# Optimization experiments

Measured on AMD Instinct MI355X. Metric: run time of the kernel, lower is better.

Reference implementation:

```python
import jax, jax.numpy as jnp
import numpy as np

B, N_DET, N_T, NY, NX = 4, 128, 2048, 256, 256


def setup_inputs() -> dict:
    key = jax.random.key(0)
    k1, k2, k3 = jax.random.split(key, 3)
    sino = jax.random.normal(k1, (B, 1, N_DET, N_T), dtype=jnp.float32)
    # LUT channel 0: floor temporal index (stored as float, cast to int in forward)
    k_floor = jax.random.randint(k2, (NY, NX, N_DET), 0, N_T).astype(jnp.float32)
    # LUT channel 1: linear interpolation weight alpha in [0,1)
    alpha = jax.random.uniform(k3, (NY, NX, N_DET), dtype=jnp.float32)
    lut = jnp.stack([k_floor, alpha], axis=-1)  # [NY, NX, N_DET, 2]
    return {"sino": sino, "lut": lut}


def reference(sino, lut):
    # sino: [B, 1, n_det, n_t]; lut: [ny, nx, n_det, 2]
    b, c, n_det, n_t = sino.shape
    k_floor = lut[..., 0].astype(jnp.int32)          # [ny, nx, n_det]
    alpha = lut[..., 1]                               # [ny, nx, n_det]
    valid = (k_floor >= 0) & (k_floor < n_t - 1)
    k0 = jnp.clip(k_floor, 0, n_t - 2)
    k1 = k0 + 1
    S = sino[:, 0]                                    # [B, n_det, n_t]
    det = jnp.arange(n_det)                           # broadcasts against [ny,nx,n_det]
    s0 = S[:, det, k0]                                # [B, ny, nx, n_det]
    s1 = S[:, det, k1]                                # [B, ny, nx, n_det]
    sk = (1.0 - alpha) * s0 + alpha * s1
    sk = jnp.where(valid, sk, jnp.zeros_like(sk))
    # Hann apodization window over detectors
    apod = (0.5 - 0.5 * jnp.cos(2.0 * jnp.pi * jnp.arange(n_det, dtype=jnp.float32)
                                / max(n_det - 1, 1))).astype(sino.dtype)
    out = jnp.einsum('bijd,d->bij', sk, apod)
    norm = jnp.maximum(apod.sum(), 1e-06)
    out = out / norm
    return out[:, None]                               # [B, 1, ny, nx]
```

## Files before the change

kernel.cpp:

```cpp
#include <hip/hip_runtime.h>
#include <hip/hip_fp16.h>


#define NB      4
#define NDET    128
#define NT      2048
#define NPIX    65536
#define THREADS 256

__global__ __launch_bounds__(256)
void cvt_kernel(const float* __restrict__ sino, uint2* __restrict__ ws16) {
    const int id = blockIdx.x * 256 + threadIdx.x;
    float v0 = sino[id];
    float v1 = sino[id + NDET * NT];
    float v2 = sino[id + 2 * NDET * NT];
    float v3 = sino[id + 3 * NDET * NT];
    __half2 h01 = __floats2half2_rn(v0, v1);
    __half2 h23 = __floats2half2_rn(v2, v3);
    uint2 u;
    u.x = *(const unsigned*)&h01;
    u.y = *(const unsigned*)&h23;
    ws16[id] = u;
}

__global__ __launch_bounds__(THREADS, 4)
void bp_kernel(const uint2* __restrict__ ws16,
               const float* __restrict__ lut,
               float* __restrict__ out) {
    const int tid    = threadIdx.x;
    const int lane   = tid & 63;
    const int wid    = tid >> 6;
    const int octet  = lane & 15;
    const int px_sub = lane >> 4;
    const int px     = blockIdx.x * 16 + wid * 4 + px_sub;
    const int d0     = octet * 8;

    float apod[8];
#pragma unroll
    for (int j = 0; j < 8; ++j) {
        float x = (float)(d0 + j) * (6.28318530717958647692f / 127.0f);
        apod[j] = 0.5f - 0.5f * __cosf(x);
    }

    const float4* lp = (const float4*)lut + ((size_t)px * 64 + octet * 4);
    float4 L[4];
#pragma unroll
    for (int q = 0; q < 4; ++q) L[q] = lp[q];

    float acc[NB] = {0.0f, 0.0f, 0.0f, 0.0f};
#pragma unroll
    for (int q = 0; q < 4; ++q) {
#pragma unroll
        for (int h = 0; h < 2; ++h) {
            int   j  = q * 2 + h;
            float kf = h ? L[q].z : L[q].x;
            float af = h ? L[q].w : L[q].y;
            int k = (int)kf;
            bool valid = (unsigned)k < (unsigned)(NT - 1);
            float w  = valid ? apod[j] : 0.0f;
            int  k0  = valid ? k : 0;
            const uint2* row = ws16 + (size_t)(d0 + j) * NT + k0;
            uint2 e0 = row[0];
            uint2 e1 = row[1];
            __half2 a01 = *(__half2*)&e0.x, a23 = *(__half2*)&e0.y;
            __half2 b01 = *(__half2*)&e1.x, b23 = *(__half2*)&e1.y;
            __half2 a2  = __float2half2_rn(af);
            __half2 s01 = __hfma2(a2, __hsub2(b01, a01), a01);
            __half2 s23 = __hfma2(a2, __hsub2(b23, a23), a23);
            float2 f01 = __half22float2(s01);
            float2 f23 = __half22float2(s23);
            acc[0] = fmaf(w, f01.x, acc[0]);
            acc[1] = fmaf(w, f01.y, acc[1]);
            acc[2] = fmaf(w, f23.x, acc[2]);
            acc[3] = fmaf(w, f23.y, acc[3]);
        }
    }

#pragma unroll
    for (int m = 1; m < 16; m <<= 1) {
#pragma unroll
        for (int b = 0; b < NB; ++b)
            acc[b] += __shfl_xor(acc[b], m, 64);
    }

    if (octet == 0) {
        const float inv_norm = 1.0f / 63.5f;
#pragma unroll
        for (int b = 0; b < NB; ++b)
            out[(size_t)b * NPIX + px] = acc[b] * inv_norm;
    }
}

__global__ __launch_bounds__(512, 4)
void bp_fallback(const float* __restrict__ sino,
                 const float* __restrict__ lut,
                 float* __restrict__ out) {
    __shared__ __half2 lds[4][NT];
    const int tid   = threadIdx.x;
    const int octet = blockIdx.x & 15;
    const int tile  = blockIdx.x >> 4;
    const int d0    = octet * 8;
    const int px0   = tile * 1024;
    float apod[8];
#pragma unroll
    for (int j = 0; j < 8; ++j) {
        float x = (float)(d0 + j) * (6.28318530717958647692f / 127.0f);
        apod[j] = 0.5f - 0.5f * __cosf(x);
    }
    float4 L[2][4];
#pragma unroll
    for (int i = 0; i < 2; ++i) {
        const float4* lq = (const float4*)
            (lut + ((size_t)(px0 + tid + i * 512) * NDET + d0) * 2);
#pragma unroll
        for (int q = 0; q < 4; ++q) L[i][q] = lq[q];
    }
    float acc[2][NB];
#pragma unroll
    for (int i = 0; i < 2; ++i)
#pragma unroll
        for (int b = 0; b < NB; ++b) acc[i][b] = 0.0f;
    const float4* s4 = (const float4*)sino;
    for (int ph = 0; ph < 4; ++ph) {
        const int b0  = (ph >> 1) * 2;
        const int dh  = ph & 1;
        const int dg0 = d0 + dh * 4;
        if (ph) __syncthreads();
        for (int f = tid; f < 4 * (NT / 4); f += 512) {
            int dl = f >> 9;
            int t4 = f & 511;
            size_t row = ((size_t)b0 * NDET + dg0 + dl) * (NT / 4) + t4;
            float4 ve = s4[row];
            float4 vo = s4[row + (size_t)NDET * (NT / 4)];
            __half2* dstp = &lds[dl][t4 * 4];
            dstp[0] = __floats2half2_rn(ve.x, vo.x);
            dstp[1] = __floats2half2_rn(ve.y, vo.y);
            dstp[2] = __floats2half2_rn(ve.z, vo.z);
            dstp[3] = __floats2half2_rn(ve.w, vo.w);
        }
        __syncthreads();
#pragma unroll
        for (int i = 0; i < 2; ++i) {
#pragma unroll
            for (int q2 = 0; q2 < 2; ++q2) {
                float4 Lq = L[i][dh * 2 + q2];
#pragma unroll
                for (int h = 0; h < 2; ++h) {
                    float kf = h ? Lq.z : Lq.x;
                    float af = h ? Lq.w : Lq.y;
                    int   dl = q2 * 2 + h;
                    int k = (int)kf;
                    bool valid = (unsigned)k < (unsigned)(NT - 1);
                    float w  = valid ? apod[dh * 4 + dl] : 0.0f;
                    int  k0  = valid ? k : 0;
                    __half2 s0v = lds[dl][k0];
                    __half2 s1v = lds[dl][k0 + 1];
                    __half2 a2  = __float2half2_rn(af);
                    __half2 sk  = __hfma2(a2, __hsub2(s1v, s0v), s0v);
                    float2  fv  = __half22float2(sk);
                    acc[i][b0 + 0] = fmaf(w, fv.x, acc[i][b0 + 0]);
                    acc[i][b0 + 1] = fmaf(w, fv.y, acc[i][b0 + 1]);
                }
            }
        }
    }
    const float inv_norm = 1.0f / 63.5f;
#pragma unroll
    for (int i = 0; i < 2; ++i) {
        const int px = px0 + tid + i * 512;
#pragma unroll
        for (int b = 0; b < NB; ++b)
            atomicAdd(&out[(size_t)b * NPIX + px], acc[i][b] * inv_norm);
    }
}

extern "C" void kernel_launch(void* const* d_in, const int* in_sizes, int n_in,
                              void* d_out, int out_size, void* d_ws, size_t ws_size,
                              hipStream_t stream) {
    const float* sino = (const float*)d_in[0];
    const float* lut  = (const float*)d_in[1];
    float* out = (float*)d_out;

    const size_t ws_needed = (size_t)NDET * NT * sizeof(uint2);
    if (ws_size >= ws_needed) {
        uint2* ws16 = (uint2*)d_ws;
        cvt_kernel<<<dim3(NDET * NT / 256), dim3(256), 0, stream>>>(sino, ws16);
        bp_kernel<<<dim3(NPIX / 16), dim3(THREADS), 0, stream>>>(ws16, lut, out);
    } else {
        (void)hipMemsetAsync(d_out, 0, (size_t)out_size * sizeof(float), stream);
        bp_fallback<<<dim3(1024), dim3(512), 0, stream>>>(sino, lut, out);
    }
}
```

Before: 125.9 us.

## Stage per-quad sinogram rows in LDS and accumulate detector partials atomically

The backprojection kernel is restructured so each 1024-thread block owns 4 detectors and a 4096-pixel tile. It first copies those detectors' fp16-packed sinogram rows (64KB) into shared memory, then performs the interpolation gathers from LDS instead of from global memory. Partial sums from the 32 detector groups are combined with float atomicAdd into an output that is zeroed by a memset beforehand. This replaces the warp-shuffle reduction. It aims to turn scattered L2 gathers into LDS gathers, at the cost of many atomics, a large LDS footprint that limits occupancy, and strided LUT reads.

Measured after the change: 144.3 us. +14.6%, slower.

```diff
diff --git a/kernel.cpp b/kernel.cpp
--- a/kernel.cpp
+++ b/kernel.cpp
@@ -6,7 +6,10 @@
 #define NDET    128
 #define NT      2048
 #define NPIX    65536
-#define THREADS 256
+#define QDET    4
+#define THREADS 1024
+#define PXTILE  4096
+#define ITERS   (PXTILE / THREADS)
 
 __global__ __launch_bounds__(256)
 void cvt_kernel(const float* __restrict__ sino, uint2* __restrict__ ws16) {
@@ -27,67 +30,69 @@
 void bp_kernel(const uint2* __restrict__ ws16,
                const float* __restrict__ lut,
                float* __restrict__ out) {
-    const int tid    = threadIdx.x;
-    const int lane   = tid & 63;
-    const int wid    = tid >> 6;
-    const int octet  = lane & 15;
-    const int px_sub = lane >> 4;
-    const int px     = blockIdx.x * 16 + wid * 4 + px_sub;
-    const int d0     = octet * 8;
+    __shared__ uint2 lds2[QDET * NT];
 
-    float apod[8];
+    const int tid  = threadIdx.x;
+    const int quad = blockIdx.x & 31;
+    const int tile = blockIdx.x >> 5;
+    const int d0   = quad * QDET;
+    const int px0  = tile * PXTILE;
+
+    float apod[QDET];
 #pragma unroll
-    for (int j = 0; j < 8; ++j) {
+    for (int j = 0; j < QDET; ++j) {
         float x = (float)(d0 + j) * (6.28318530717958647692f / 127.0f);
         apod[j] = 0.5f - 0.5f * __cosf(x);
     }
 
-    const float4* lp = (const float4*)lut + ((size_t)px * 64 + octet * 4);
-    float4 L[4];
+    {
+        const uint4* src = (const uint4*)(ws16 + (size_t)d0 * NT);
+        uint4* dst = (uint4*)lds2;
 #pragma unroll
-    for (int q = 0; q < 4; ++q) L[q] = lp[q];
+        for (int r = 0; r < (QDET * NT / 2) / THREADS; ++r)
+            dst[tid + r * THREADS] = src[tid + r * THREADS];
+    }
+    __syncthreads();
 
-    float acc[NB] = {0.0f, 0.0f, 0.0f, 0.0f};
+    const float inv_norm = 1.0f / 63.5f;
+
+    for (int it = 0; it < ITERS; ++it) {
+        const int px = px0 + it * THREADS + tid;
+        const float4* lp = (const float4*)(lut + ((size_t)px * NDET + d0) * 2);
+        float4 L0 = lp[0];
+        float4 L1 = lp[1];
+
+        float acc[NB] = {0.0f, 0.0f, 0.0f, 0.0f};
 #pragma unroll
-    for (int q = 0; q < 4; ++q) {
+        for (int q = 0; q < 2; ++q) {
+            float4 Lq = q ? L1 : L0;
 #pragma unroll
-        for (int h = 0; h < 2; ++h) {
-            int   j  = q * 2 + h;
-            float kf = h ? L[q].z : L[q].x;
-            float af = h ? L[q].w : L[q].y;
-            int k = (int)kf;
-            bool valid = (unsigned)k < (unsigned)(NT - 1);
-            float w  = valid ? apod[j] : 0.0f;
-            int  k0  = valid ? k : 0;
-            const uint2* row = ws16 + (size_t)(d0 + j) * NT + k0;
-            uint2 e0 = row[0];
-            uint2 e1 = row[1];
-            __half2 a01 = *(__half2*)&e0.x, a23 = *(__half2*)&e0.y;
-            __half2 b01 = *(__half2*)&e1.x, b23 = *(__half2*)&e1.y;
-            __half2 a2  = __float2half2_rn(af);
-            __half2 s01 = __hfma2(a2, __hsub2(b01, a01), a01);
-            __half2 s23 = __hfma2(a2, __hsub2(b23, a23), a23);
-            float2 f01 = __half22float2(s01);
-            float2 f23 = __half22float2(s23);
-            acc[0] = fmaf(w, f01.x, acc[0]);
-            acc[1] = fmaf(w, f01.y, acc[1]);
-            acc[2] = fmaf(w, f23.x, acc[2]);
-            acc[3] = fmaf(w, f23.y, acc[3]);
+            for (int h = 0; h < 2; ++h) {
+                int   j  = q * 2 + h;
+                float kf = h ? Lq.z : Lq.x;
+                float af = h ? Lq.w : Lq.y;
+                int k = (int)kf;
+                bool valid = (unsigned)k < (unsigned)(NT - 1);
+                float w  = valid ? apod[j] : 0.0f;
+                int  k0  = valid ? k : 0;
+                uint2 e0 = lds2[j * NT + k0];
+                uint2 e1 = lds2[j * NT + k0 + 1];
+                __half2 a01 = *(__half2*)&e0.x, a23 = *(__half2*)&e0.y;
+                __half2 b01 = *(__half2*)&e1.x, b23 = *(__half2*)&e1.y;
+                __half2 a2  = __float2half2_rn(af);
+                __half2 s01 = __hfma2(a2, __hsub2(b01, a01), a01);
+                __half2 s23 = __hfma2(a2, __hsub2(b23, a23), a23);
+                float2 f01 = __half22float2(s01);
+                float2 f23 = __half22float2(s23);
+                acc[0] = fmaf(w, f01.x, acc[0]);
+                acc[1] = fmaf(w, f01.y, acc[1]);
+                acc[2] = fmaf(w, f23.x, acc[2]);
+                acc[3] = fmaf(w, f23.y, acc[3]);
+            }
         }
-    }
-
-#pragma unroll
-    for (int m = 1; m < 16; m <<= 1) {
 #pragma unroll
         for (int b = 0; b < NB; ++b)
-            acc[b] += __shfl_xor(acc[b], m, 64);
-    }
-
-    if (octet == 0) {
-        const float inv_norm = 1.0f / 63.5f;
-#pragma unroll
-        for (int b = 0; b < NB; ++b)
-            out[(size_t)b * NPIX + px] = acc[b] * inv_norm;
+            atomicAdd(&out[(size_t)b * NPIX + px], acc[b] * inv_norm);
     }
 }
 
@@ -181,13 +186,14 @@
     const float* lut  = (const float*)d_in[1];
     float* out = (float*)d_out;
 
+    (void)hipMemsetAsync(d_out, 0, (size_t)out_size * sizeof(float), stream);
+
     const size_t ws_needed = (size_t)NDET * NT * sizeof(uint2);
     if (ws_size >= ws_needed) {
         uint2* ws16 = (uint2*)d_ws;
         cvt_kernel<<<dim3(NDET * NT / 256), dim3(256), 0, stream>>>(sino, ws16);
-        bp_kernel<<<dim3(NPIX / 16), dim3(THREADS), 0, stream>>>(ws16, lut, out);
+        bp_kernel<<<dim3(512), dim3(THREADS), 0, stream>>>(ws16, lut, out);
     } else {
-        (void)hipMemsetAsync(d_out, 0, (size_t)out_size * sizeof(float), stream);
         bp_fallback<<<dim3(1024), dim3(512), 0, stream>>>(sino, lut, out);
     }
 }
```
